# Performance work log

Measured on AMD Instinct MI355X. Metric: run time of the kernel, lower is better.

Reference implementation:

```python
import jax, jax.numpy as jnp
import numpy as np

FP8_MAX = 448.0          # E4M3 max representable
SAFETY_MARGIN = 1.1
SCALE_CAP = 10000.0


def _fp8_scale(t):
    """Per-tensor dynamic scale (single step: tracked amax == current amax)."""
    amax = jax.lax.stop_gradient(jnp.max(jnp.abs(t)))
    scale = FP8_MAX / (amax * SAFETY_MARGIN)
    scale = jnp.where(amax == 0.0, 1.0, jnp.minimum(scale, SCALE_CAP))
    return scale


def _quantize_e4m3(t, scale):
    """Scale, clamp to E4M3 range, round to fp8, return dequantized-to-fp32 codes."""
    ts = jnp.clip(t * scale, -FP8_MAX, FP8_MAX)
    return ts.astype(jnp.float8_e4m3fn).astype(jnp.float32)


def setup_inputs() -> dict:
    key = jax.random.key(0)
    k1, k2, k3 = jax.random.split(key, 3)
    B, S, D_IN, D_OUT = 4, 2048, 4096, 4096
    x = jax.random.normal(k1, (B, S, D_IN), dtype=jnp.float32)
    weight = jax.random.normal(k2, (D_OUT, D_IN), dtype=jnp.float32) * 0.02
    bias = jax.random.normal(k3, (D_OUT,), dtype=jnp.float32) * 0.02
    return {"x": x, "weight": weight, "bias": bias}


def reference(x, weight, bias):
    orig_shape = x.shape
    x2 = x.reshape(-1, orig_shape[-1])               # [M, d_in]

    x_scale = _fp8_scale(x2)
    w_scale = _fp8_scale(weight)

    x_fp8 = _quantize_e4m3(x2, x_scale)              # fp8 codes held in fp32
    w_fp8 = _quantize_e4m3(weight, w_scale)

    # torch._scaled_mm: out = (x_fp8 @ w_fp8^T) * scale_a * scale_b, scale_* = 1/scale
    out = jnp.einsum('mk,nk->mn', x_fp8, w_fp8) * (1.0 / x_scale) * (1.0 / w_scale)
    out = out.reshape(*orig_shape[:-1], out.shape[-1])
    out = out + bias
    return out
```

## Files before the change

kernel.cpp:

```cpp
#include <hip/hip_runtime.h>
#include <hip/hip_bf16.h>

typedef float f32x16 __attribute__((ext_vector_type(16)));
typedef int   i32x8  __attribute__((ext_vector_type(8)));
typedef int   i32x4  __attribute__((ext_vector_type(4)));

#define FP8_MAX 448.0f


__device__ __forceinline__ void g2l16(const void* g, void* l) {
    __builtin_amdgcn_global_load_lds(
        (const __attribute__((address_space(1))) void*)g,
        (__attribute__((address_space(3))) void*)l,
        16, 0, 0);
}

__device__ __forceinline__ float scale_from(float amax) {
    float s = FP8_MAX / (amax * 1.1f);
    return (amax == 0.0f) ? 1.0f : fminf(s, 10000.0f);
}


__global__ void init_kernel(unsigned* amax) {
    amax[0] = 0u;
    amax[1] = 0u;
}

__global__ void amax_fused_kernel(const float* __restrict__ x, size_t nx,
                                  const float* __restrict__ w, size_t nw,
                                  unsigned* __restrict__ amax, int xblocks) {
    const float* src;
    size_t n;
    unsigned* out;
    int bid, nb;
    if ((int)blockIdx.x < xblocks) {
        src = x; n = nx; out = amax; bid = blockIdx.x; nb = xblocks;
    } else {
        src = w; n = nw; out = amax + 1; bid = blockIdx.x - xblocks; nb = gridDim.x - xblocks;
    }
    float m = 0.0f;
    const size_t ustep = (size_t)blockDim.x * 4;
    const size_t chunkf = ustep * 8;
    size_t base = (size_t)bid * chunkf + (size_t)threadIdx.x * 4;
    const size_t gstride = (size_t)nb * chunkf;
    for (; base < n; base += gstride) {
        float4 v[8];
        #pragma unroll
        for (int u = 0; u < 8; ++u) {
            size_t idx = base + (size_t)u * ustep;
            float4 vv = {0.0f, 0.0f, 0.0f, 0.0f};
            if (idx < n) vv = *(const float4*)(src + idx);
            v[u] = vv;
        }
        #pragma unroll
        for (int u = 0; u < 8; ++u)
            m = fmaxf(m, fmaxf(fmaxf(fabsf(v[u].x), fabsf(v[u].y)),
                               fmaxf(fabsf(v[u].z), fabsf(v[u].w))));
    }
    #pragma unroll
    for (int off = 32; off > 0; off >>= 1)
        m = fmaxf(m, __shfl_xor(m, off));
    __shared__ float sm[4];
    if ((threadIdx.x & 63) == 0) sm[threadIdx.x >> 6] = m;
    __syncthreads();
    if (threadIdx.x == 0) {
        float mm = fmaxf(fmaxf(sm[0], sm[1]), fmaxf(sm[2], sm[3]));
        atomicMax(out, __float_as_uint(mm));
    }
}

__device__ __forceinline__ float qclamp(float v, float s) {
    return fminf(fmaxf(v * s, -FP8_MAX), FP8_MAX);
}

__global__ void quant_fused_kernel(const float* __restrict__ x, size_t nx,
                                   const float* __restrict__ w, size_t nw,
                                   const unsigned* __restrict__ amax,
                                   unsigned char* __restrict__ xq,
                                   unsigned char* __restrict__ wq, int xblocks) {
    const float* src;
    size_t n;
    unsigned char* dst;
    int bid, nb, sel;
    if ((int)blockIdx.x < xblocks) {
        src = x; n = nx; dst = xq; bid = blockIdx.x; nb = xblocks; sel = 0;
    } else {
        src = w; n = nw; dst = wq; bid = blockIdx.x - xblocks; nb = gridDim.x - xblocks; sel = 1;
    }
    const float s = scale_from(__uint_as_float(amax[sel]));
    const size_t ustep = (size_t)blockDim.x * 4;
    const size_t chunkf = ustep * 4;
    size_t base = (size_t)bid * chunkf + (size_t)threadIdx.x * 4;
    const size_t gstride = (size_t)nb * chunkf;
    for (; base < n; base += gstride) {
        float4 v[4];
        bool ok[4];
        #pragma unroll
        for (int u = 0; u < 4; ++u) {
            size_t idx = base + (size_t)u * ustep;
            ok[u] = idx < n;
            float4 vv = {0.0f, 0.0f, 0.0f, 0.0f};
            if (ok[u]) vv = *(const float4*)(src + idx);
            v[u] = vv;
        }
        #pragma unroll
        for (int u = 0; u < 4; ++u) {
            if (ok[u]) {
                int p = __builtin_amdgcn_cvt_pk_fp8_f32(qclamp(v[u].x, s), qclamp(v[u].y, s), 0, false);
                p = __builtin_amdgcn_cvt_pk_fp8_f32(qclamp(v[u].z, s), qclamp(v[u].w, s), p, true);
                *(unsigned*)(dst + base + (size_t)u * ustep) = (unsigned)p;
            }
        }
    }
}

#define BM 128
#define BN 256
#define BKB 128

__global__ __launch_bounds__(256, 2) void gemm_fp8_kernel(
    const unsigned char* __restrict__ Aq,
    const unsigned char* __restrict__ Bq,
    const float* __restrict__ bias,
    const unsigned* __restrict__ amax,
    float* __restrict__ out,
    int M, int N, int K) {
    __shared__ alignas(16) unsigned char sA[BM * BKB];
    __shared__ alignas(16) unsigned char sB[BN * BKB];

    const int tid = threadIdx.x;
    const int wave = tid >> 6;
    const int lane = tid & 63;
    const int nbn = N / BN;
    const int brow = (blockIdx.x / nbn) * BM;
    const int bcol = (blockIdx.x % nbn) * BN;
    const int wrow = (wave >> 1) * 64;
    const int wcol = (wave & 1) * 128;

    f32x16 acc[2][4] = {};

    const int r31 = lane & 31;
    const int half = lane >> 5;
    const int so = tid * 16;

    union AB { i32x8 v8; i32x4 v4[2]; };

    for (int k0 = 0; k0 < K; k0 += BKB) {
        __syncthreads();
        #pragma unroll
        for (int i = 0; i < 4; ++i) {
            int oo = i * 4096 + so;
            int r = oo >> 7;
            int cl = (oo & 127) ^ ((r & 7) << 4);
            g2l16(Aq + (size_t)(brow + r) * K + k0 + cl, &sA[i * 4096 + wave * 1024]);
        }
        #pragma unroll
        for (int i = 0; i < 8; ++i) {
            int oo = i * 4096 + so;
            int r = oo >> 7;
            int cl = (oo & 127) ^ ((r & 7) << 4);
            g2l16(Bq + (size_t)(bcol + r) * K + k0 + cl, &sB[i * 4096 + wave * 1024]);
        }
        __syncthreads();

        #pragma unroll
        for (int ks = 0; ks < 2; ++ks) {
            const int kb = ks * 64 + half * 32;
            AB a[2], b[4];
            #pragma unroll
            for (int m = 0; m < 2; ++m) {
                int row = wrow + m * 32 + r31;
                int bse = row * BKB;
                int sw = (row & 7) << 4;
                a[m].v4[0] = *(const i32x4*)&sA[bse + (kb ^ sw)];
                a[m].v4[1] = *(const i32x4*)&sA[bse + ((kb + 16) ^ sw)];
            }
            #pragma unroll
            for (int n = 0; n < 4; ++n) {
                int row = wcol + n * 32 + r31;
                int bse = row * BKB;
                int sw = (row & 7) << 4;
                b[n].v4[0] = *(const i32x4*)&sB[bse + (kb ^ sw)];
                b[n].v4[1] = *(const i32x4*)&sB[bse + ((kb + 16) ^ sw)];
            }
            #pragma unroll
            for (int m = 0; m < 2; ++m)
                #pragma unroll
                for (int n = 0; n < 4; ++n)
                    acc[m][n] = __builtin_amdgcn_mfma_scale_f32_32x32x64_f8f6f4(
                        a[m].v8, b[n].v8, acc[m][n],
                        0, 0, 0, 0x7f7f7f7f, 0, 0x7f7f7f7f);
        }
    }

    const float invx = 1.0f / scale_from(__uint_as_float(amax[0]));
    const float invw = 1.0f / scale_from(__uint_as_float(amax[1]));
    #pragma unroll
    for (int n = 0; n < 4; ++n) {
        int col = bcol + wcol + n * 32 + r31;
        float bv = bias[col];
        #pragma unroll
        for (int m = 0; m < 2; ++m) {
            int rbase = brow + wrow + m * 32 + half * 4;
            #pragma unroll
            for (int r = 0; r < 16; ++r) {
                int row = rbase + (r & 3) + 8 * (r >> 2);
                out[(size_t)row * N + col] = acc[m][n][r] * invx * invw + bv;
            }
        }
    }
}


extern "C" void kernel_launch(void* const* d_in, const int* in_sizes, int n_in,
                              void* d_out, int out_size, void* d_ws, size_t ws_size,
                              hipStream_t stream) {
    const float* x    = (const float*)d_in[0];
    const float* w    = (const float*)d_in[1];
    const float* bias = (const float*)d_in[2];
    float* out = (float*)d_out;

    const size_t nx = (size_t)in_sizes[0];
    const size_t nw = (size_t)in_sizes[1];
    const int N = in_sizes[2];
    const int K = (int)(nw / (size_t)N);
    const int M = (int)(nx / (size_t)K);

    unsigned* amax = (unsigned*)d_ws;
    unsigned char* xq = (unsigned char*)d_ws + 256;
    unsigned char* wq = xq + nx;

    const int TOTB = 2048;
    int xb = (int)((double)TOTB * (double)nx / (double)(nx + nw));
    if (xb < 1) xb = 1;
    if (xb > TOTB - 1) xb = TOTB - 1;

    init_kernel<<<1, 1, 0, stream>>>(amax);
    amax_fused_kernel<<<TOTB, 256, 0, stream>>>(x, nx, w, nw, amax, xb);
    quant_fused_kernel<<<TOTB, 256, 0, stream>>>(x, nx, w, nw, amax, xq, wq, xb);

    dim3 grid((M / BM) * (N / BN));
    gemm_fp8_kernel<<<grid, 256, 0, stream>>>(xq, wq, bias, amax, out, M, N, K);
}
```

Baseline: 216.4 us.

## Rewrite FP8 GEMM as 256x256 double-buffered ping-pong pipeline with XCD remap

The GEMM moves to 256x256 tiles with 512 threads and double-buffered LDS. Global-to-LDS loads for the next K tile are interleaved with MFMA quarter-steps using explicit barriers, waitcnt and setprio. This is meant to hide memory latency behind compute and improve reuse per block. Block IDs are also remapped across the 8 XCDs for L2 locality. In exchange, LDS use per block rises to 128KB, which limits occupancy to one block per CU, and the hand-tuned vmcnt counts are fragile.

Measured after the change: 248.8 us. 15.0% more time.

```diff
diff --git a/kernel.cpp b/kernel.cpp
--- a/kernel.cpp
+++ b/kernel.cpp
@@ -114,101 +114,239 @@
     }
 }
 
-#define BM 128
+#define BM 256
 #define BN 256
 #define BKB 128
 
-__global__ __launch_bounds__(256, 2) void gemm_fp8_kernel(
+__global__ __launch_bounds__(512) void gemm_fp8_kernel(
     const unsigned char* __restrict__ Aq,
     const unsigned char* __restrict__ Bq,
     const float* __restrict__ bias,
     const unsigned* __restrict__ amax,
     float* __restrict__ out,
     int M, int N, int K) {
-    __shared__ alignas(16) unsigned char sA[BM * BKB];
-    __shared__ alignas(16) unsigned char sB[BN * BKB];
+    __shared__ alignas(16) unsigned char sA[2][BM * BKB];
+    __shared__ alignas(16) unsigned char sB[2][BN * BKB];
 
     const int tid = threadIdx.x;
     const int wave = tid >> 6;
     const int lane = tid & 63;
-    const int nbn = N / BN;
-    const int brow = (blockIdx.x / nbn) * BM;
-    const int bcol = (blockIdx.x % nbn) * BN;
-    const int wrow = (wave >> 1) * 64;
-    const int wcol = (wave & 1) * 128;
-
-    f32x16 acc[2][4] = {};
-
     const int r31 = lane & 31;
     const int half = lane >> 5;
-    const int so = tid * 16;
-
-    union AB { i32x8 v8; i32x4 v4[2]; };
-
-    for (int k0 = 0; k0 < K; k0 += BKB) {
-        __syncthreads();
-        #pragma unroll
-        for (int i = 0; i < 4; ++i) {
-            int oo = i * 4096 + so;
+    const int sw = (r31 & 7) << 4;
+
+    int nwg = (int)gridDim.x;
+    int bid = (int)blockIdx.x;
+    if ((nwg & 7) == 0) {
+        int cpx = nwg >> 3;
+        bid = (bid & 7) * cpx + (bid >> 3);
+    }
+    const int nbn = N / BN;
+    const int brow = (bid / nbn) * BM;
+    const int bcol = (bid % nbn) * BN;
+
+    const int R0 = (wave >> 2) * 128;
+    const int C0 = (wave & 3) * 64;
+
+    f32x16 acc[4][2] = {};
+
+    const int NT = K / BKB;
+    const int NI = NT / 2;
+    const int j0 = tid * 16;
+
+    auto stageA = [&](int buf, int h, int t) {
+        #pragma unroll
+        for (int j = 0; j < 2; ++j) {
+            int oo = j * 8192 + j0;
             int r = oo >> 7;
             int cl = (oo & 127) ^ ((r & 7) << 4);
-            g2l16(Aq + (size_t)(brow + r) * K + k0 + cl, &sA[i * 4096 + wave * 1024]);
-        }
-        #pragma unroll
-        for (int i = 0; i < 8; ++i) {
-            int oo = i * 4096 + so;
+            g2l16(Aq + (size_t)(brow + h * 128 + r) * K + t * BKB + cl,
+                  &sA[buf][h * 16384 + j * 8192 + wave * 1024]);
+        }
+    };
+    auto stageB = [&](int buf, int h, int t) {
+        #pragma unroll
+        for (int j = 0; j < 2; ++j) {
+            int oo = j * 8192 + j0;
             int r = oo >> 7;
             int cl = (oo & 127) ^ ((r & 7) << 4);
-            g2l16(Bq + (size_t)(bcol + r) * K + k0 + cl, &sB[i * 4096 + wave * 1024]);
-        }
-        __syncthreads();
-
-        #pragma unroll
-        for (int ks = 0; ks < 2; ++ks) {
-            const int kb = ks * 64 + half * 32;
-            AB a[2], b[4];
-            #pragma unroll
-            for (int m = 0; m < 2; ++m) {
-                int row = wrow + m * 32 + r31;
-                int bse = row * BKB;
-                int sw = (row & 7) << 4;
-                a[m].v4[0] = *(const i32x4*)&sA[bse + (kb ^ sw)];
-                a[m].v4[1] = *(const i32x4*)&sA[bse + ((kb + 16) ^ sw)];
-            }
-            #pragma unroll
-            for (int n = 0; n < 4; ++n) {
-                int row = wcol + n * 32 + r31;
-                int bse = row * BKB;
-                int sw = (row & 7) << 4;
-                b[n].v4[0] = *(const i32x4*)&sB[bse + (kb ^ sw)];
-                b[n].v4[1] = *(const i32x4*)&sB[bse + ((kb + 16) ^ sw)];
-            }
-            #pragma unroll
-            for (int m = 0; m < 2; ++m)
-                #pragma unroll
-                for (int n = 0; n < 4; ++n)
-                    acc[m][n] = __builtin_amdgcn_mfma_scale_f32_32x32x64_f8f6f4(
-                        a[m].v8, b[n].v8, acc[m][n],
-                        0, 0, 0, 0x7f7f7f7f, 0, 0x7f7f7f7f);
-        }
+            g2l16(Bq + (size_t)(bcol + h * 128 + r) * K + t * BKB + cl,
+                  &sB[buf][h * 16384 + j * 8192 + wave * 1024]);
+        }
+    };
+    auto rdA = [&](int buf, int row, int ks) -> i32x8 {
+        const unsigned char* base = &sA[buf][row * BKB];
+        int kb = ks * 64 + half * 32;
+        union { i32x8 v8; i32x4 v4[2]; } u;
+        u.v4[0] = *(const i32x4*)(base + (kb ^ sw));
+        u.v4[1] = *(const i32x4*)(base + ((kb + 16) ^ sw));
+        return u.v8;
+    };
+    auto rdB = [&](int buf, int row, int ks) -> i32x8 {
+        const unsigned char* base = &sB[buf][row * BKB];
+        int kb = ks * 64 + half * 32;
+        union { i32x8 v8; i32x4 v4[2]; } u;
+        u.v4[0] = *(const i32x4*)(base + (kb ^ sw));
+        u.v4[1] = *(const i32x4*)(base + ((kb + 16) ^ sw));
+        return u.v8;
+    };
+
+    #define MM(a, b, c) \
+        c = __builtin_amdgcn_mfma_scale_f32_32x32x64_f8f6f4( \
+            a, b, c, 0, 0, 0, 0x7f7f7f7f, 0, 0x7f7f7f7f)
+    #define BARRIER()  __builtin_amdgcn_s_barrier()
+    #define LGKM0()    asm volatile("s_waitcnt lgkmcnt(0)" ::: "memory")
+    #define VMCNT2()   asm volatile("s_waitcnt vmcnt(2)" ::: "memory")
+
+    stageA(0, 0, 0); stageA(0, 1, 0); stageB(0, 0, 0); stageB(0, 1, 0);
+    stageA(1, 0, 1);
+    VMCNT2();
+    BARRIER();
+
+    for (int I = 0; I < NI; ++I) {
+        const int u = 2 * I;
+        const int v = u + 1;
+        const int t2 = (u + 2 < NT) ? u + 2 : 0;
+        const int v2 = (v + 2 < NT) ? v + 2 : 0;
+
+        i32x8 a0[2][2], a1[2][2], b0[2], b1[2];
+
+        #pragma unroll
+        for (int f = 0; f < 2; ++f)
+            #pragma unroll
+            for (int ks = 0; ks < 2; ++ks)
+                a0[f][ks] = rdA(0, R0 + f * 32 + r31, ks);
+        #pragma unroll
+        for (int ks = 0; ks < 2; ++ks) b0[ks] = rdB(0, C0 + r31, ks);
+        stageA(1, 1, v);
+        BARRIER(); LGKM0();
+        __builtin_amdgcn_s_setprio(1);
+        #pragma unroll
+        for (int f = 0; f < 2; ++f)
+            #pragma unroll
+            for (int ks = 0; ks < 2; ++ks) MM(a0[f][ks], b0[ks], acc[f][0]);
+        __builtin_amdgcn_s_setprio(0);
+        BARRIER();
+
+        #pragma unroll
+        for (int ks = 0; ks < 2; ++ks) b1[ks] = rdB(0, C0 + 32 + r31, ks);
+        stageB(1, 0, v);
+        BARRIER(); LGKM0();
+        __builtin_amdgcn_s_setprio(1);
+        #pragma unroll
+        for (int f = 0; f < 2; ++f)
+            #pragma unroll
+            for (int ks = 0; ks < 2; ++ks) MM(a0[f][ks], b1[ks], acc[f][1]);
+        __builtin_amdgcn_s_setprio(0);
+        BARRIER();
+
+        #pragma unroll
+        for (int f = 0; f < 2; ++f)
+            #pragma unroll
+            for (int ks = 0; ks < 2; ++ks)
+                a1[f][ks] = rdA(0, R0 + 64 + f * 32 + r31, ks);
+        stageB(1, 1, v);
+        BARRIER(); LGKM0();
+        __builtin_amdgcn_s_setprio(1);
+        #pragma unroll
+        for (int f = 0; f < 2; ++f)
+            #pragma unroll
+            for (int ks = 0; ks < 2; ++ks) MM(a1[f][ks], b1[ks], acc[2 + f][1]);
+        __builtin_amdgcn_s_setprio(0);
+        BARRIER();
+
+        #pragma unroll
+        for (int ks = 0; ks < 2; ++ks) b0[ks] = rdB(0, C0 + r31, ks);
+        stageA(0, 0, t2);
+        VMCNT2();
+        BARRIER(); LGKM0();
+        __builtin_amdgcn_s_setprio(1);
+        #pragma unroll
+        for (int f = 0; f < 2; ++f)
+            #pragma unroll
+            for (int ks = 0; ks < 2; ++ks) MM(a1[f][ks], b0[ks], acc[2 + f][0]);
+        __builtin_amdgcn_s_setprio(0);
+        BARRIER();
+
+        #pragma unroll
+        for (int f = 0; f < 2; ++f)
+            #pragma unroll
+            for (int ks = 0; ks < 2; ++ks)
+                a0[f][ks] = rdA(1, R0 + f * 32 + r31, ks);
+        #pragma unroll
+        for (int ks = 0; ks < 2; ++ks) b0[ks] = rdB(1, C0 + r31, ks);
+        stageA(0, 1, t2);
+        BARRIER(); LGKM0();
+        __builtin_amdgcn_s_setprio(1);
+        #pragma unroll
+        for (int f = 0; f < 2; ++f)
+            #pragma unroll
+            for (int ks = 0; ks < 2; ++ks) MM(a0[f][ks], b0[ks], acc[f][0]);
+        __builtin_amdgcn_s_setprio(0);
+        BARRIER();
+
+        #pragma unroll
+        for (int ks = 0; ks < 2; ++ks) b1[ks] = rdB(1, C0 + 32 + r31, ks);
+        stageB(0, 0, t2);
+        BARRIER(); LGKM0();
+        __builtin_amdgcn_s_setprio(1);
+        #pragma unroll
+        for (int f = 0; f < 2; ++f)
+            #pragma unroll
+            for (int ks = 0; ks < 2; ++ks) MM(a0[f][ks], b1[ks], acc[f][1]);
+        __builtin_amdgcn_s_setprio(0);
+        BARRIER();
+
+        #pragma unroll
+        for (int f = 0; f < 2; ++f)
+            #pragma unroll
+            for (int ks = 0; ks < 2; ++ks)
+                a1[f][ks] = rdA(1, R0 + 64 + f * 32 + r31, ks);
+        stageB(0, 1, t2);
+        BARRIER(); LGKM0();
+        __builtin_amdgcn_s_setprio(1);
+        #pragma unroll
+        for (int f = 0; f < 2; ++f)
+            #pragma unroll
+            for (int ks = 0; ks < 2; ++ks) MM(a1[f][ks], b1[ks], acc[2 + f][1]);
+        __builtin_amdgcn_s_setprio(0);
+        BARRIER();
+
+        #pragma unroll
+        for (int ks = 0; ks < 2; ++ks) b0[ks] = rdB(1, C0 + r31, ks);
+        stageA(1, 0, v2);
+        VMCNT2();
+        BARRIER(); LGKM0();
+        __builtin_amdgcn_s_setprio(1);
+        #pragma unroll
+        for (int f = 0; f < 2; ++f)
+            #pragma unroll
+            for (int ks = 0; ks < 2; ++ks) MM(a1[f][ks], b0[ks], acc[2 + f][0]);
+        __builtin_amdgcn_s_setprio(0);
+        BARRIER();
     }
 
     const float invx = 1.0f / scale_from(__uint_as_float(amax[0]));
     const float invw = 1.0f / scale_from(__uint_as_float(amax[1]));
+    const float s2 = invx * invw;
     #pragma unroll
-    for (int n = 0; n < 4; ++n) {
-        int col = bcol + wcol + n * 32 + r31;
+    for (int n = 0; n < 2; ++n) {
+        int col = bcol + C0 + n * 32 + r31;
         float bv = bias[col];
         #pragma unroll
-        for (int m = 0; m < 2; ++m) {
-            int rbase = brow + wrow + m * 32 + half * 4;
+        for (int m = 0; m < 4; ++m) {
+            int rbase = brow + R0 + m * 32 + half * 4;
             #pragma unroll
             for (int r = 0; r < 16; ++r) {
                 int row = rbase + (r & 3) + 8 * (r >> 2);
-                out[(size_t)row * N + col] = acc[m][n][r] * invx * invw + bv;
+                out[(size_t)row * N + col] = acc[m][n][r] * s2 + bv;
             }
         }
     }
+    #undef MM
+    #undef BARRIER
+    #undef LGKM0
+    #undef VMCNT2
 }
 
 
@@ -240,5 +378,5 @@
     quant_fused_kernel<<<TOTB, 256, 0, stream>>>(x, nx, w, nw, amax, xq, wq, xb);
 
     dim3 grid((M / BM) * (N / BN));
-    gemm_fp8_kernel<<<grid, 256, 0, stream>>>(xq, wq, bias, amax, out, M, N, K);
-}
+    gemm_fp8_kernel<<<grid, 512, 0, stream>>>(xq, wq, bias, amax, out, M, N, K);
+}
```

## Rebuild FP8 GEMM as 256x256 tile with 4-stage LDS pipeline and XCD remap

Applied to the files above, without the earlier changes.

Restructures the FP8 GEMM to use 512 threads per block with 256x256 output tiles and K-step 64. It keeps a 4-slot shared-memory ring with three tiles prefetched through async global-to-LDS loads, so memory traffic overlaps the MFMA work. It also remaps block IDs so neighbouring tiles land on the same XCD, and raises wave priority during the MFMA section. The cost is more LDS per block (128KB, which likely drops occupancy to one block per CU) and a more complex barrier and waitcnt protocol. At the end of K the loop wraps around and issues redundant prefetch loads.

Measured after the change: 236.0 us. 1.09x slower.

```diff
diff --git a/kernel.cpp b/kernel.cpp
--- a/kernel.cpp
+++ b/kernel.cpp
@@ -114,101 +114,139 @@
     }
 }
 
-#define BM 128
+#define BM 256
 #define BN 256
-#define BKB 128
-
-__global__ __launch_bounds__(256, 2) void gemm_fp8_kernel(
+#define BKB 64
+
+__global__ __launch_bounds__(512, 2) void gemm_fp8_kernel(
     const unsigned char* __restrict__ Aq,
     const unsigned char* __restrict__ Bq,
     const float* __restrict__ bias,
     const unsigned* __restrict__ amax,
     float* __restrict__ out,
     int M, int N, int K) {
-    __shared__ alignas(16) unsigned char sA[BM * BKB];
-    __shared__ alignas(16) unsigned char sB[BN * BKB];
+    __shared__ alignas(16) unsigned char sA[4][BM * BKB];
+    __shared__ alignas(16) unsigned char sB[4][BN * BKB];
 
     const int tid = threadIdx.x;
     const int wave = tid >> 6;
     const int lane = tid & 63;
-    const int nbn = N / BN;
-    const int brow = (blockIdx.x / nbn) * BM;
-    const int bcol = (blockIdx.x % nbn) * BN;
-    const int wrow = (wave >> 1) * 64;
-    const int wcol = (wave & 1) * 128;
-
-    f32x16 acc[2][4] = {};
-
     const int r31 = lane & 31;
     const int half = lane >> 5;
-    const int so = tid * 16;
-
-    union AB { i32x8 v8; i32x4 v4[2]; };
-
-    for (int k0 = 0; k0 < K; k0 += BKB) {
-        __syncthreads();
-        #pragma unroll
-        for (int i = 0; i < 4; ++i) {
-            int oo = i * 4096 + so;
-            int r = oo >> 7;
-            int cl = (oo & 127) ^ ((r & 7) << 4);
-            g2l16(Aq + (size_t)(brow + r) * K + k0 + cl, &sA[i * 4096 + wave * 1024]);
-        }
-        #pragma unroll
-        for (int i = 0; i < 8; ++i) {
-            int oo = i * 4096 + so;
-            int r = oo >> 7;
-            int cl = (oo & 127) ^ ((r & 7) << 4);
-            g2l16(Bq + (size_t)(bcol + r) * K + k0 + cl, &sB[i * 4096 + wave * 1024]);
-        }
-        __syncthreads();
-
-        #pragma unroll
-        for (int ks = 0; ks < 2; ++ks) {
-            const int kb = ks * 64 + half * 32;
-            AB a[2], b[4];
+
+    int nwg = (int)gridDim.x;
+    int bid = (int)blockIdx.x;
+    if ((nwg & 7) == 0) {
+        int cpx = nwg >> 3;
+        bid = (bid & 7) * cpx + (bid >> 3);
+    }
+    const int nbn = N / BN;
+    const int brow = (bid / nbn) * BM;
+    const int bcol = (bid % nbn) * BN;
+
+    const int R0 = (wave >> 2) * 128;
+    const int C0 = (wave & 3) * 64;
+
+    f32x16 acc[4][2] = {};
+
+    const int NT = K / BKB;
+    const int j0 = tid * 16;
+
+    auto stageA = [&](int slot, int t) {
+        #pragma unroll
+        for (int j = 0; j < 2; ++j) {
+            int oo = j * 8192 + j0;
+            int r = oo >> 6;
+            int c = (oo & 63) ^ (((r >> 1) & 3) << 4);
+            g2l16(Aq + (size_t)(brow + r) * K + t * BKB + c,
+                  &sA[slot][j * 8192 + wave * 1024]);
+        }
+    };
+    auto stageB = [&](int slot, int t) {
+        #pragma unroll
+        for (int j = 0; j < 2; ++j) {
+            int oo = j * 8192 + j0;
+            int r = oo >> 6;
+            int c = (oo & 63) ^ (((r >> 1) & 3) << 4);
+            g2l16(Bq + (size_t)(bcol + r) * K + t * BKB + c,
+                  &sB[slot][j * 8192 + wave * 1024]);
+        }
+    };
+    auto rdA = [&](int slot, int row) -> i32x8 {
+        const unsigned char* base = &sA[slot][row * BKB];
+        int swz = ((row >> 1) & 3) << 4;
+        int kb = half * 32;
+        union { i32x8 v8; i32x4 v4[2]; } u;
+        u.v4[0] = *(const i32x4*)(base + (kb ^ swz));
+        u.v4[1] = *(const i32x4*)(base + ((kb + 16) ^ swz));
+        return u.v8;
+    };
+    auto rdB = [&](int slot, int row) -> i32x8 {
+        const unsigned char* base = &sB[slot][row * BKB];
+        int swz = ((row >> 1) & 3) << 4;
+        int kb = half * 32;
+        union { i32x8 v8; i32x4 v4[2]; } u;
+        u.v4[0] = *(const i32x4*)(base + (kb ^ swz));
+        u.v4[1] = *(const i32x4*)(base + ((kb + 16) ^ swz));
+        return u.v8;
+    };
+
+    #define MM(a, b, c) \
+        c = __builtin_amdgcn_mfma_scale_f32_32x32x64_f8f6f4( \
+            a, b, c, 0, 0, 0, 0x7f7f7f7f, 0, 0x7f7f7f7f)
+
+    stageA(0, 0); stageB(0, 0);
+    stageA(1, 1); stageB(1, 1);
+    stageA(2, 2); stageB(2, 2);
+    asm volatile("s_waitcnt vmcnt(8)" ::: "memory");
+    __builtin_amdgcn_s_barrier();
+
+    for (int t = 0; t < NT; ++t) {
+        const int s = t & 3;
+        i32x8 a[4], b[2];
+        #pragma unroll
+        for (int m = 0; m < 4; ++m) a[m] = rdA(s, R0 + m * 32 + r31);
+        #pragma unroll
+        for (int n = 0; n < 2; ++n) b[n] = rdB(s, C0 + n * 32 + r31);
+
+        int tt = t + 3;
+        if (tt >= NT) tt -= NT;
+        stageA(tt & 3, tt);
+        stageB(tt & 3, tt);
+
+        asm volatile("s_waitcnt vmcnt(8)" ::: "memory");
+        __builtin_amdgcn_s_barrier();
+        asm volatile("s_waitcnt lgkmcnt(0)" ::: "memory");
+        __builtin_amdgcn_sched_barrier(0);
+
+        __builtin_amdgcn_s_setprio(1);
+        #pragma unroll
+        for (int m = 0; m < 4; ++m)
             #pragma unroll
-            for (int m = 0; m < 2; ++m) {
-                int row = wrow + m * 32 + r31;
-                int bse = row * BKB;
-                int sw = (row & 7) << 4;
-                a[m].v4[0] = *(const i32x4*)&sA[bse + (kb ^ sw)];
-                a[m].v4[1] = *(const i32x4*)&sA[bse + ((kb + 16) ^ sw)];
-            }
-            #pragma unroll
-            for (int n = 0; n < 4; ++n) {
-                int row = wcol + n * 32 + r31;
-                int bse = row * BKB;
-                int sw = (row & 7) << 4;
-                b[n].v4[0] = *(const i32x4*)&sB[bse + (kb ^ sw)];
-                b[n].v4[1] = *(const i32x4*)&sB[bse + ((kb + 16) ^ sw)];
-            }
-            #pragma unroll
-            for (int m = 0; m < 2; ++m)
-                #pragma unroll
-                for (int n = 0; n < 4; ++n)
-                    acc[m][n] = __builtin_amdgcn_mfma_scale_f32_32x32x64_f8f6f4(
-                        a[m].v8, b[n].v8, acc[m][n],
-                        0, 0, 0, 0x7f7f7f7f, 0, 0x7f7f7f7f);
-        }
+            for (int n = 0; n < 2; ++n)
+                MM(a[m], b[n], acc[m][n]);
+        __builtin_amdgcn_s_setprio(0);
+        __builtin_amdgcn_s_barrier();
     }
 
     const float invx = 1.0f / scale_from(__uint_as_float(amax[0]));
     const float invw = 1.0f / scale_from(__uint_as_float(amax[1]));
+    const float s2 = invx * invw;
     #pragma unroll
-    for (int n = 0; n < 4; ++n) {
-        int col = bcol + wcol + n * 32 + r31;
+    for (int n = 0; n < 2; ++n) {
+        int col = bcol + C0 + n * 32 + r31;
         float bv = bias[col];
         #pragma unroll
-        for (int m = 0; m < 2; ++m) {
-            int rbase = brow + wrow + m * 32 + half * 4;
+        for (int m = 0; m < 4; ++m) {
+            int rbase = brow + R0 + m * 32 + half * 4;
             #pragma unroll
             for (int r = 0; r < 16; ++r) {
                 int row = rbase + (r & 3) + 8 * (r >> 2);
-                out[(size_t)row * N + col] = acc[m][n][r] * invx * invw + bv;
+                out[(size_t)row * N + col] = acc[m][n][r] * s2 + bv;
             }
         }
     }
+    #undef MM
 }
 
 
@@ -240,5 +278,5 @@
     quant_fused_kernel<<<TOTB, 256, 0, stream>>>(x, nx, w, nw, amax, xq, wq, xb);
 
     dim3 grid((M / BM) * (N / BN));
-    gemm_fp8_kernel<<<grid, 256, 0, stream>>>(xq, wq, bias, amax, out, M, N, K);
-}
+    gemm_fp8_kernel<<<grid, 512, 0, stream>>>(xq, wq, bias, amax, out, M, N, K);
+}
```

## Load GEMM A-operand directly from global into registers, bypassing LDS

Applied to the files above, without the earlier changes.

Removes the shared-memory tile for the quantized activations and has each lane load its A fragments directly from global memory into registers, while B still goes through LDS. This is meant to cut LDS footprint and LDS read traffic for A. In exchange, A loads are non-prefetched global reads with strided row access and duplicated across waves sharing rows, exposing latency. Also folds the two dequant scales into one multiplier in the epilogue.

Result: slower. 264.2 us (+22.1%).

```diff
diff --git a/kernel.cpp b/kernel.cpp
--- a/kernel.cpp
+++ b/kernel.cpp
@@ -125,7 +125,6 @@
     const unsigned* __restrict__ amax,
     float* __restrict__ out,
     int M, int N, int K) {
-    __shared__ alignas(16) unsigned char sA[BM * BKB];
     __shared__ alignas(16) unsigned char sB[BN * BKB];
 
     const int tid = threadIdx.x;
@@ -145,15 +144,14 @@
 
     union AB { i32x8 v8; i32x4 v4[2]; };
 
+    const size_t sK = (size_t)K;
+    const unsigned char* ap[2];
+    #pragma unroll
+    for (int m = 0; m < 2; ++m)
+        ap[m] = Aq + (size_t)(brow + wrow + m * 32 + r31) * sK + half * 32;
+
     for (int k0 = 0; k0 < K; k0 += BKB) {
         __syncthreads();
-        #pragma unroll
-        for (int i = 0; i < 4; ++i) {
-            int oo = i * 4096 + so;
-            int r = oo >> 7;
-            int cl = (oo & 127) ^ ((r & 7) << 4);
-            g2l16(Aq + (size_t)(brow + r) * K + k0 + cl, &sA[i * 4096 + wave * 1024]);
-        }
         #pragma unroll
         for (int i = 0; i < 8; ++i) {
             int oo = i * 4096 + so;
@@ -161,20 +159,21 @@
             int cl = (oo & 127) ^ ((r & 7) << 4);
             g2l16(Bq + (size_t)(bcol + r) * K + k0 + cl, &sB[i * 4096 + wave * 1024]);
         }
+        AB a[2][2];
+        #pragma unroll
+        for (int m = 0; m < 2; ++m)
+            #pragma unroll
+            for (int ks = 0; ks < 2; ++ks) {
+                const unsigned char* p = ap[m] + k0 + ks * 64;
+                a[m][ks].v4[0] = *(const i32x4*)(p);
+                a[m][ks].v4[1] = *(const i32x4*)(p + 16);
+            }
         __syncthreads();
 
         #pragma unroll
         for (int ks = 0; ks < 2; ++ks) {
             const int kb = ks * 64 + half * 32;
-            AB a[2], b[4];
-            #pragma unroll
-            for (int m = 0; m < 2; ++m) {
-                int row = wrow + m * 32 + r31;
-                int bse = row * BKB;
-                int sw = (row & 7) << 4;
-                a[m].v4[0] = *(const i32x4*)&sA[bse + (kb ^ sw)];
-                a[m].v4[1] = *(const i32x4*)&sA[bse + ((kb + 16) ^ sw)];
-            }
+            AB b[4];
             #pragma unroll
             for (int n = 0; n < 4; ++n) {
                 int row = wcol + n * 32 + r31;
@@ -188,13 +187,14 @@
                 #pragma unroll
                 for (int n = 0; n < 4; ++n)
                     acc[m][n] = __builtin_amdgcn_mfma_scale_f32_32x32x64_f8f6f4(
-                        a[m].v8, b[n].v8, acc[m][n],
+                        a[m][ks].v8, b[n].v8, acc[m][n],
                         0, 0, 0, 0x7f7f7f7f, 0, 0x7f7f7f7f);
         }
     }
 
     const float invx = 1.0f / scale_from(__uint_as_float(amax[0]));
     const float invw = 1.0f / scale_from(__uint_as_float(amax[1]));
+    const float s2 = invx * invw;
     #pragma unroll
     for (int n = 0; n < 4; ++n) {
         int col = bcol + wcol + n * 32 + r31;
@@ -205,7 +205,7 @@
             #pragma unroll
             for (int r = 0; r < 16; ++r) {
                 int row = rbase + (r & 3) + 8 * (r >> 2);
-                out[(size_t)row * N + col] = acc[m][n][r] * invx * invw + bv;
+                out[(size_t)row * N + col] = acc[m][n][r] * s2 + bv;
             }
         }
     }
```
